# Kernel tuning notes

Measured on AMD Instinct MI355X. Metric: run time of the kernel, lower is better.

## Reference

```python
import jax, jax.numpy as jnp
import numpy as np
from functools import partial

TAU_MEM = 10.0
TAU_SYN = (5.0, 10.0)
THRESHOLD = 1.0
WINDOW = 0.3
BATCH = 32
T = 256
N_SYN = 2
N_NEURONS = 2048


@jax.custom_vjp
def spike_fn(v_shifted):
    # Heaviside of (vmem - threshold); surrogate gradient is a boxcar of width `window`.
    return (v_shifted > 0).astype(v_shifted.dtype)


def _spike_fwd(v_shifted):
    return spike_fn(v_shifted), v_shifted


def _spike_bwd(v_shifted, g):
    surr = (jnp.abs(v_shifted) < WINDOW).astype(g.dtype) / WINDOW
    return (g * surr,)


spike_fn.defvjp(_spike_fwd, _spike_bwd)


def setup_inputs() -> dict:
    key = jax.random.key(0)
    # Poisson-like analog spike input, shape (batch*T, n_syn, n_neurons)
    binary_input = (jax.random.uniform(key, (BATCH * T, N_SYN, N_NEURONS), dtype=jnp.float32) < 0.1
                    ).astype(jnp.float32)
    return {"binary_input": binary_input}


def reference(binary_input):
    # (B*T, n_syn, N) -> (B, T, n_syn, N) -> time-major, synapse-last: (T, B, N, n_syn)
    x = binary_input.reshape(BATCH, T, N_SYN, N_NEURONS).transpose(1, 0, 3, 2)

    alpha_mem = jnp.exp(jnp.float32(-1.0 / TAU_MEM))
    alpha_syn = jnp.exp(-1.0 / jnp.asarray(TAU_SYN, dtype=jnp.float32))  # [n_syn]

    def step(carry, inp_t):
        vmem, isyn = carry                      # vmem [B,N], isyn [B,N,n_syn]
        isyn = alpha_syn * isyn + inp_t         # leaky synaptic integration
        vmem = alpha_mem * vmem + isyn.sum(-1)  # leaky membrane integration
        spikes = spike_fn(vmem - THRESHOLD)     # threshold crossing
        vmem = vmem - spikes * THRESHOLD        # reset by subtraction
        return (vmem, isyn), spikes

    v0 = jnp.zeros((BATCH, N_NEURONS), dtype=x.dtype)
    i0 = jnp.zeros((BATCH, N_NEURONS, N_SYN), dtype=x.dtype)
    _, all_spikes = jax.lax.scan(step, (v0, i0), x)  # [T, B, N]

    # back to (batch*T, N) as in the torch module's trailing reshape
    return all_spikes.transpose(1, 0, 2).reshape(-1, N_NEURONS)
```

## Files before the change

kernel.cpp:

```cpp
#include <hip/hip_runtime.h>
#include <math.h>

#define T_STEPS   256
#define N_NEUR    2048
#define N_BATCH   32

#define CHUNK   16
#define NCHUNK  (T_STEPS / CHUNK)


__global__ __launch_bounds__(256) void snn_scan_kernel(
    const float* __restrict__ in,
    float* __restrict__ out,
    float a_mem, float a_s0, float a_s1)
{
    const int tid = blockIdx.x * blockDim.x + threadIdx.x;
    const int n = tid & (N_NEUR - 1);
    const int b = tid >> 11;

    const float* pin = in + (size_t)b * T_STEPS * 2 * N_NEUR + n;
    float* pout      = out + (size_t)b * T_STEPS * N_NEUR + n;

    float vmem = 0.0f;
    float i0 = 0.0f;
    float i1 = 0.0f;

    float xa0[CHUNK], xb0[CHUNK];
    float xa1[CHUNK], xb1[CHUNK];

#define LOADC(XA, XB, CIDX)                                                  \
    {                                                                        \
        const float* p_ = pin + (size_t)(CIDX) * CHUNK * (2 * N_NEUR);       \
        _Pragma("unroll")                                                    \
        for (int k = 0; k < CHUNK; ++k) {                                    \
            XA[k] = p_[(size_t)k * (2 * N_NEUR)];                            \
            XB[k] = p_[(size_t)k * (2 * N_NEUR) + N_NEUR];                   \
        }                                                                    \
    }

#define COMPUTEC(XA, XB, CIDX)                                               \
    {                                                                        \
        float* po_ = pout + (size_t)(CIDX) * CHUNK * N_NEUR;                 \
        _Pragma("unroll")                                                    \
        for (int k = 0; k < CHUNK; ++k) {                                    \
            i0 = __fadd_rn(__fmul_rn(a_s0, i0), XA[k]);                      \
            i1 = __fadd_rn(__fmul_rn(a_s1, i1), XB[k]);                      \
            const float ssum = __fadd_rn(i0, i1);                            \
            vmem = __fadd_rn(__fmul_rn(a_mem, vmem), ssum);                  \
            const float vs = __fsub_rn(vmem, 1.0f);                          \
            const bool fired = (vs > 0.0f);                                  \
            po_[(size_t)k * N_NEUR] = fired ? 1.0f : 0.0f;                   \
            vmem = fired ? vs : vmem;                                        \
        }                                                                    \
    }

    LOADC(xa0, xb0, 0);
    LOADC(xa1, xb1, 1);

    for (int c = 0; c < NCHUNK; c += 2) {
        COMPUTEC(xa0, xb0, c);
        if (c + 2 < NCHUNK) LOADC(xa0, xb0, c + 2);
        COMPUTEC(xa1, xb1, c + 1);
        if (c + 3 < NCHUNK) LOADC(xa1, xb1, c + 3);
    }

#undef LOADC
#undef COMPUTEC
}

extern "C" void kernel_launch(void* const* d_in, const int* in_sizes, int n_in,
                              void* d_out, int out_size, void* d_ws, size_t ws_size,
                              hipStream_t stream) {
    const float* in = (const float*)d_in[0];
    float* out = (float*)d_out;

    const float a_s0  = (float)exp((double)(-1.0f / 5.0f));
    const float a_s1  = (float)exp((double)(-1.0f / 10.0f));
    const float a_mem = (float)exp((double)(-1.0f / 10.0f));

    const int total_threads = N_BATCH * N_NEUR;
    dim3 block(256);
    dim3 grid(total_threads / 256);

    snn_scan_kernel<<<grid, block, 0, stream>>>(in, out, a_mem, a_s0, a_s1);
}
```

Before: 211.4 us.

## Process two neurons per thread with vectorized nontemporal loads and stores

Each thread now handles two adjacent neurons, using 8-byte vector loads and stores with nontemporal hints, and the chunk size and block size are halved. The aim is to cut the number of memory instructions and avoid cache pollution for streaming data. The cost is half as many threads (32K total, 256 blocks of 128), which reduces latency hiding and the occupancy available to this latency-bound sequential scan.

```diff
diff --git a/kernel.cpp b/kernel.cpp
--- a/kernel.cpp
+++ b/kernel.cpp
@@ -5,36 +5,40 @@
 #define N_NEUR    2048
 #define N_BATCH   32
 
-#define CHUNK   16
+#define CHUNK   8
 #define NCHUNK  (T_STEPS / CHUNK)
 
+typedef float f32x2 __attribute__((ext_vector_type(2)));
 
-__global__ __launch_bounds__(256) void snn_scan_kernel(
+
+__global__ __launch_bounds__(128) void snn_scan_kernel(
     const float* __restrict__ in,
     float* __restrict__ out,
     float a_mem, float a_s0, float a_s1)
 {
     const int tid = blockIdx.x * blockDim.x + threadIdx.x;
-    const int n = tid & (N_NEUR - 1);
-    const int b = tid >> 11;
+    const int n2 = tid & (N_NEUR / 2 - 1);
+    const int b  = tid >> 10;
 
-    const float* pin = in + (size_t)b * T_STEPS * 2 * N_NEUR + n;
-    float* pout      = out + (size_t)b * T_STEPS * N_NEUR + n;
+    const float* pin = in + (size_t)b * T_STEPS * 2 * N_NEUR + 2 * n2;
+    float* pout      = out + (size_t)b * T_STEPS * N_NEUR + 2 * n2;
 
-    float vmem = 0.0f;
-    float i0 = 0.0f;
-    float i1 = 0.0f;
+    f32x2 vmem = {0.0f, 0.0f};
+    f32x2 i0   = {0.0f, 0.0f};
+    f32x2 i1   = {0.0f, 0.0f};
 
-    float xa0[CHUNK], xb0[CHUNK];
-    float xa1[CHUNK], xb1[CHUNK];
+    f32x2 xa0[CHUNK], xb0[CHUNK];
+    f32x2 xa1[CHUNK], xb1[CHUNK];
 
 #define LOADC(XA, XB, CIDX)                                                  \
     {                                                                        \
         const float* p_ = pin + (size_t)(CIDX) * CHUNK * (2 * N_NEUR);       \
         _Pragma("unroll")                                                    \
         for (int k = 0; k < CHUNK; ++k) {                                    \
-            XA[k] = p_[(size_t)k * (2 * N_NEUR)];                            \
-            XB[k] = p_[(size_t)k * (2 * N_NEUR) + N_NEUR];                   \
+            XA[k] = __builtin_nontemporal_load(                              \
+                (const f32x2*)(p_ + (size_t)k * (2 * N_NEUR)));              \
+            XB[k] = __builtin_nontemporal_load(                              \
+                (const f32x2*)(p_ + (size_t)k * (2 * N_NEUR) + N_NEUR));     \
         }                                                                    \
     }
 
@@ -43,14 +47,27 @@
         float* po_ = pout + (size_t)(CIDX) * CHUNK * N_NEUR;                 \
         _Pragma("unroll")                                                    \
         for (int k = 0; k < CHUNK; ++k) {                                    \
-            i0 = __fadd_rn(__fmul_rn(a_s0, i0), XA[k]);                      \
-            i1 = __fadd_rn(__fmul_rn(a_s1, i1), XB[k]);                      \
-            const float ssum = __fadd_rn(i0, i1);                            \
-            vmem = __fadd_rn(__fmul_rn(a_mem, vmem), ssum);                  \
-            const float vs = __fsub_rn(vmem, 1.0f);                          \
-            const bool fired = (vs > 0.0f);                                  \
-            po_[(size_t)k * N_NEUR] = fired ? 1.0f : 0.0f;                   \
-            vmem = fired ? vs : vmem;                                        \
+            const f32x2 x0 = XA[k];                                          \
+            const f32x2 x1 = XB[k];                                          \
+            i0.x = __fadd_rn(__fmul_rn(a_s0, i0.x), x0.x);                   \
+            i0.y = __fadd_rn(__fmul_rn(a_s0, i0.y), x0.y);                   \
+            i1.x = __fadd_rn(__fmul_rn(a_s1, i1.x), x1.x);                   \
+            i1.y = __fadd_rn(__fmul_rn(a_s1, i1.y), x1.y);                   \
+            const float sx = __fadd_rn(i0.x, i1.x);                          \
+            const float sy = __fadd_rn(i0.y, i1.y);                          \
+            vmem.x = __fadd_rn(__fmul_rn(a_mem, vmem.x), sx);                \
+            vmem.y = __fadd_rn(__fmul_rn(a_mem, vmem.y), sy);                \
+            const float vsx = __fsub_rn(vmem.x, 1.0f);                       \
+            const float vsy = __fsub_rn(vmem.y, 1.0f);                       \
+            const bool fx = (vsx > 0.0f);                                    \
+            const bool fy = (vsy > 0.0f);                                    \
+            f32x2 sp;                                                        \
+            sp.x = fx ? 1.0f : 0.0f;                                         \
+            sp.y = fy ? 1.0f : 0.0f;                                         \
+            __builtin_nontemporal_store(                                     \
+                sp, (f32x2*)(po_ + (size_t)k * N_NEUR));                     \
+            vmem.x = fx ? vsx : vmem.x;                                      \
+            vmem.y = fy ? vsy : vmem.y;                                      \
         }                                                                    \
     }
 
@@ -78,9 +95,9 @@
     const float a_s1  = (float)exp((double)(-1.0f / 10.0f));
     const float a_mem = (float)exp((double)(-1.0f / 10.0f));
 
-    const int total_threads = N_BATCH * N_NEUR;
-    dim3 block(256);
-    dim3 grid(total_threads / 256);
+    const int total_threads = N_BATCH * N_NEUR / 2;
+    dim3 block(128);
+    dim3 grid(total_threads / 128);
 
     snn_scan_kernel<<<grid, block, 0, stream>>>(in, out, a_mem, a_s0, a_s1);
 }
```

New measurement: 211.4 us. Within noise of the previous version (-0.0%).
